# Performance work log

Hardware: AMD Instinct MI355X
Metric: run time of the kernel (lower is better)

The kernel has to match this reference:

```python
import jax, jax.numpy as jnp
import numpy as np

N = 16384       # pedestrian_num
D_IN = 2        # input_size
H = 64          # hidden_size


def setup_inputs() -> dict:
    key = jax.random.key(0)
    ks = jax.random.split(key, 4)
    data = jax.random.normal(ks[0], (N, D_IN), dtype=jnp.float32)
    # Linear weights stored as [in, out]; scaled like torch default init (~1/sqrt(in)).
    W1 = jax.random.normal(ks[1], (D_IN, 32), dtype=jnp.float32) / np.sqrt(D_IN)
    b1 = jnp.zeros((32,), dtype=jnp.float32)
    W2 = jax.random.normal(ks[2], (32, 64), dtype=jnp.float32) / np.sqrt(32)
    b2 = jnp.zeros((64,), dtype=jnp.float32)
    W3 = jax.random.normal(ks[3], (64, H), dtype=jnp.float32) / np.sqrt(64)
    b3 = jnp.zeros((H,), dtype=jnp.float32)
    return {"data": data, "W1": W1, "b1": b1, "W2": W2, "b2": b2, "W3": W3, "b3": b3}


def reference(data, W1, b1, W2, b2, W3, b3):
    # Per-pedestrian MLP (batched over all N pedestrians at once).
    h = jax.nn.relu(data @ W1 + b1)          # [N, 32]
    h = jax.nn.relu(h @ W2 + b2)             # [N, 64]
    h = h @ W3 + b3                          # [N, H]
    # Spatial affinity: the original fills the lower triangle with <h_i, h_j>
    # and its softmax reads entry [max(i,j), min(i,j)], i.e. the full
    # symmetric Gram matrix G = h @ h.T.
    G = jnp.einsum("nd,md->nm", h, h)        # [N, N], symmetric
    # Row-wise softmax over the symmetric affinity matrix.
    return jax.nn.softmax(G, axis=-1)
```

## Files before the change

### kernel.cpp

```cpp
#include <hip/hip_runtime.h>

#define N     16384
#define DH    64
#define TILE  128
#define NT    (N / TILE)
#define S2    133

typedef __attribute__((ext_vector_type(8))) short  short8;
typedef __attribute__((ext_vector_type(4))) float  f32x4;

__device__ __forceinline__ ushort bf_hi(float x) {
    unsigned u = __float_as_uint(x);
    unsigned r = u + 0x7FFFu + ((u >> 16) & 1u);
    return (ushort)(r >> 16);
}
__device__ __forceinline__ float bf_val(ushort h) {
    return __uint_as_float(((unsigned)h) << 16);
}

__device__ __forceinline__ short8 ldfrag(const ushort* __restrict__ p, int row, int koff) {
    return *(const short8*)(p + (size_t)row * DH + koff);
}

__global__ __launch_bounds__(128) void mlp_kernel(
    const float* __restrict__ data,
    const float* __restrict__ W1, const float* __restrict__ b1,
    const float* __restrict__ W2, const float* __restrict__ b2,
    const float* __restrict__ W3, const float* __restrict__ b3,
    ushort* __restrict__ hHi, ushort* __restrict__ hLo)
{
    __shared__ float sW1[64], sb1[32], sW2[32 * 64], sb2[64], sW3[64 * 64], sb3[64];
    const int tid = threadIdx.x;
    if (tid < 64) sW1[tid] = W1[tid];
    if (tid < 32) sb1[tid] = b1[tid];
    if (tid < 64) sb2[tid] = b2[tid];
    if (tid < 64) sb3[tid] = b3[tid];
    for (int t = tid; t < 32 * 64; t += 128) sW2[t] = W2[t];
    for (int t = tid; t < 64 * 64; t += 128) sW3[t] = W3[t];
    __syncthreads();

    const int i = blockIdx.x * 128 + tid;
    const float x0 = data[2 * i + 0];
    const float x1 = data[2 * i + 1];

    float h1[32];
#pragma unroll
    for (int o = 0; o < 32; ++o)
        h1[o] = fmaxf(0.f, fmaf(x0, sW1[o], fmaf(x1, sW1[32 + o], sb1[o])));

    float h2[64];
#pragma unroll
    for (int o = 0; o < 64; ++o) {
        float a = sb2[o];
#pragma unroll
        for (int k = 0; k < 32; ++k) a = fmaf(h1[k], sW2[k * 64 + o], a);
        h2[o] = fmaxf(0.f, a);
    }

    ushort hs[64], ls[64];
#pragma unroll
    for (int o = 0; o < 64; ++o) {
        float a = sb3[o];
#pragma unroll
        for (int k = 0; k < 64; ++k) a = fmaf(h2[k], sW3[k * 64 + o], a);
        const ushort hb = bf_hi(a);
        hs[o] = hb;
        ls[o] = bf_hi(a - bf_val(hb));
    }
#pragma unroll
    for (int q = 0; q < 8; ++q) {
        short8 vh, vl;
#pragma unroll
        for (int t = 0; t < 8; ++t) { vh[t] = (short)hs[q * 8 + t]; vl[t] = (short)ls[q * 8 + t]; }
        *(short8*)(hHi + (size_t)i * DH + q * 8) = vh;
        *(short8*)(hLo + (size_t)i * DH + q * 8) = vl;
    }
}

__device__ __forceinline__ void stage_B(
    const ushort* __restrict__ hHi, const ushort* __restrict__ hLo,
    int brow0, int tid, ushort* __restrict__ sB)
{
    const int arr = tid >> 7;
    const int r   = tid & 127;
    const ushort* __restrict__ src = (arr ? hLo : hHi) + (size_t)(brow0 + r) * DH;
    ushort* __restrict__ dst = sB + arr * (TILE * DH) + r * 64;
    const int sw = (r & 7);
#pragma unroll
    for (int q = 0; q < 8; ++q) {
        const short8 v = *(const short8*)(src + q * 8);
        *(short8*)(dst + 8 * (q ^ sw)) = v;
    }
}

__device__ __forceinline__ short8 ldB(const ushort* __restrict__ sB,
                                      int arr, int row, int ks, int kb)
{
    return *(const short8*)(sB + arr * (TILE * DH) + row * 64 + 8 * (((ks << 2) + kb) ^ (row & 7)));
}

__device__ __forceinline__ void gram_tile(
    const ushort* __restrict__ hHi, const ushort* __restrict__ hLo,
    const ushort* __restrict__ sB,
    int bi, int wave, int r16, int kb, f32x4 acc[2][8])
{
#pragma unroll
    for (int rb = 0; rb < 2; ++rb)
#pragma unroll
        for (int cb = 0; cb < 8; ++cb) acc[rb][cb] = (f32x4){0.f, 0.f, 0.f, 0.f};

    const int arow = bi * TILE + wave * 16 + r16;
#pragma unroll
    for (int ks = 0; ks < 2; ++ks) {
        const int koff = ks * 32 + kb * 8;
        const short8 Ah0 = ldfrag(hHi, arow,      koff);
        const short8 Ah1 = ldfrag(hHi, arow + 64, koff);
        const short8 Al0 = ldfrag(hLo, arow,      koff);
        const short8 Al1 = ldfrag(hLo, arow + 64, koff);
#pragma unroll
        for (int cb = 0; cb < 8; ++cb) {
            const int brow = cb * 16 + r16;
            const short8 Bh = ldB(sB, 0, brow, ks, kb);
            const short8 Bl = ldB(sB, 1, brow, ks, kb);
            acc[0][cb] = __builtin_amdgcn_mfma_f32_16x16x32_bf16(Ah0, Bh, acc[0][cb], 0, 0, 0);
            acc[0][cb] = __builtin_amdgcn_mfma_f32_16x16x32_bf16(Ah0, Bl, acc[0][cb], 0, 0, 0);
            acc[0][cb] = __builtin_amdgcn_mfma_f32_16x16x32_bf16(Al0, Bh, acc[0][cb], 0, 0, 0);
            acc[1][cb] = __builtin_amdgcn_mfma_f32_16x16x32_bf16(Ah1, Bh, acc[1][cb], 0, 0, 0);
            acc[1][cb] = __builtin_amdgcn_mfma_f32_16x16x32_bf16(Ah1, Bl, acc[1][cb], 0, 0, 0);
            acc[1][cb] = __builtin_amdgcn_mfma_f32_16x16x32_bf16(Al1, Bh, acc[1][cb], 0, 0, 0);
        }
    }
}

__device__ __forceinline__ int tile_row(int wave, int kb, int rb, int reg) {
    return rb * 64 + wave * 16 + kb * 4 + reg;
}

__device__ __forceinline__ void tri_decode(int p, int& bi, int& bj) {
    const int xcd = p & 7, s = p >> 3;
    const int q = s / 129, r = s % 129;
    const int P = xcd * 8 + q;
    if (r <= P) { bi = r;         bj = P;       }
    else        { bi = r - P - 1; bj = 127 - P; }
}

#define SMEM1_BYTES 32768

__global__ __launch_bounds__(256, 4) void pass1_mfma(
    const ushort* __restrict__ hHi, const ushort* __restrict__ hLo,
    float* __restrict__ part_m, float* __restrict__ part_l)
{
    int bi, bj;
    tri_decode(blockIdx.x, bi, bj);

    __shared__ __attribute__((aligned(16))) char smem[SMEM1_BYTES];
    ushort* sB = (ushort*)smem;
    float*  jm = (float*)smem;
    float*  jl = jm + 512;

    const int tid = threadIdx.x;
    const int wave = tid >> 6, lane = tid & 63;
    const int r16 = lane & 15, kb = lane >> 4;

    stage_B(hHi, hLo, bj * TILE, tid, sB);
    __syncthreads();

    f32x4 acc[2][8];
    gram_tile(hHi, hLo, sB, bi, wave, r16, kb, acc);

#pragma unroll
    for (int rb = 0; rb < 2; ++rb) {
#pragma unroll
        for (int reg = 0; reg < 4; ++reg) {
            float m = acc[rb][0][reg];
#pragma unroll
            for (int cb = 1; cb < 8; ++cb) m = fmaxf(m, acc[rb][cb][reg]);
            m = fmaxf(m, __shfl_xor(m, 1));
            m = fmaxf(m, __shfl_xor(m, 2));
            m = fmaxf(m, __shfl_xor(m, 4));
            m = fmaxf(m, __shfl_xor(m, 8));
            float sum = 0.f;
#pragma unroll
            for (int cb = 0; cb < 8; ++cb) sum += __expf(acc[rb][cb][reg] - m);
            sum += __shfl_xor(sum, 1);
            sum += __shfl_xor(sum, 2);
            sum += __shfl_xor(sum, 4);
            sum += __shfl_xor(sum, 8);
            if (r16 == 0) {
                const int grow = bi * TILE + tile_row(wave, kb, rb, reg);
                part_m[(size_t)bj * N + grow] = m;
                part_l[(size_t)bj * N + grow] = sum;
            }
        }
    }

    if (bi != bj) {
        __syncthreads();
#pragma unroll
        for (int cb = 0; cb < 8; ++cb) {
            float m = acc[0][cb][0];
#pragma unroll
            for (int rb = 0; rb < 2; ++rb)
#pragma unroll
                for (int reg = 0; reg < 4; ++reg) m = fmaxf(m, acc[rb][cb][reg]);
            m = fmaxf(m, __shfl_xor(m, 16));
            m = fmaxf(m, __shfl_xor(m, 32));
            float sum = 0.f;
#pragma unroll
            for (int rb = 0; rb < 2; ++rb)
#pragma unroll
                for (int reg = 0; reg < 4; ++reg) sum += __expf(acc[rb][cb][reg] - m);
            sum += __shfl_xor(sum, 16);
            sum += __shfl_xor(sum, 32);
            if (kb == 0) { jm[wave * 128 + cb * 16 + r16] = m; jl[wave * 128 + cb * 16 + r16] = sum; }
        }
        __syncthreads();
        if (tid < 128) {
            float M = jm[tid];
#pragma unroll
            for (int w = 1; w < 4; ++w) M = fmaxf(M, jm[w * 128 + tid]);
            float L = 0.f;
#pragma unroll
            for (int w = 0; w < 4; ++w) L += jl[w * 128 + tid] * __expf(jm[w * 128 + tid] - M);
            part_m[(size_t)bi * N + bj * TILE + tid] = M;
            part_l[(size_t)bi * N + bj * TILE + tid] = L;
        }
    }
}

__global__ __launch_bounds__(256) void merge_kernel(
    const float* __restrict__ part_m, const float* __restrict__ part_l,
    float* __restrict__ srow)
{
    const int i = blockIdx.x * 256 + threadIdx.x;
    float M = -3.0e38f;
    for (int o = 0; o < NT; ++o) M = fmaxf(M, part_m[(size_t)o * N + i]);
    float L = 0.f;
    for (int o = 0; o < NT; ++o)
        L = fmaf(part_l[(size_t)o * N + i], __expf(part_m[(size_t)o * N + i] - M), L);
    srow[i] = M + __logf(L);
}

__global__ __launch_bounds__(256, 2) void pass2_mfma(
    const ushort* __restrict__ hHi, const ushort* __restrict__ hLo,
    const float* __restrict__ srow,
    float* __restrict__ out)
{
    const int p = blockIdx.x;
    const int xcd = p & 7, slot = p >> 3;
    const int bj  = xcd * 16 + (slot & 15);
    const int bi0 = (slot >> 4) * 16;

    const int tid = threadIdx.x;
    const int wave = tid >> 6, lane = tid & 63;
    const int r16 = lane & 15, kb = lane >> 4;

    __shared__ __attribute__((aligned(16))) ushort sB[2 * TILE * DH];
    __shared__ float ldsP[64 * S2];

    stage_B(hHi, hLo, bj * TILE, tid, sB);
    __syncthreads();

    for (int it = 0; it < 16; ++it) {
        const int bi = bi0 + it;

        f32x4 acc[2][8];
        gram_tile(hHi, hLo, sB, bi, wave, r16, kb, acc);

#pragma unroll
        for (int hh = 0; hh < 2; ++hh) {
#pragma unroll
            for (int reg = 0; reg < 4; ++reg) {
                const int rl   = wave * 16 + kb * 4 + reg;
                const int grow = bi * TILE + hh * 64 + rl;
                const float s  = srow[grow];
#pragma unroll
                for (int cb = 0; cb < 8; ++cb)
                    ldsP[rl * S2 + cb * 16 + r16] = __expf(acc[hh][cb][reg] - s);
            }
            __syncthreads();
#pragma unroll
            for (int qq = 0; qq < 8; ++qq) {
                const int f4 = tid + 256 * qq;
                const int rl = f4 >> 5, c4 = f4 & 31;
                const f32x4 v = *(const f32x4*)&ldsP[rl * S2 + c4 * 4];
                f32x4* dst = (f32x4*)(out + (size_t)(bi * TILE + hh * 64 + rl) * N + bj * TILE + c4 * 4);
                __builtin_nontemporal_store(v, dst);
            }
            __syncthreads();
        }
    }
}

extern "C" void kernel_launch(void* const* d_in, const int* in_sizes, int n_in,
                              void* d_out, int out_size, void* d_ws, size_t ws_size,
                              hipStream_t stream)
{
    const float* data = (const float*)d_in[0];
    const float* W1   = (const float*)d_in[1];
    const float* b1   = (const float*)d_in[2];
    const float* W2   = (const float*)d_in[3];
    const float* b2   = (const float*)d_in[4];
    const float* W3   = (const float*)d_in[5];
    const float* b3   = (const float*)d_in[6];
    float* out = (float*)d_out;

    float* part_m = (float*)d_ws;
    float* part_l = part_m + (size_t)NT * N;
    float* srow   = part_l + (size_t)NT * N;
    ushort* hHi   = (ushort*)(srow + 2 * N);
    ushort* hLo   = hHi + (size_t)N * DH;

    mlp_kernel<<<N / 128, 128, 0, stream>>>(data, W1, b1, W2, b2, W3, b3, hHi, hLo);
    pass1_mfma<<<NT * (NT + 1) / 2, 256, 0, stream>>>(hHi, hLo, part_m, part_l);
    merge_kernel<<<N / 256, 256, 0, stream>>>(part_m, part_l, srow);
    pass2_mfma<<<1024, 256, 0, stream>>>(hHi, hLo, srow, out);
}
```

Measured before the change: 355.8 us.

## Compute full Gram grid in pass1 instead of exploiting symmetry

Pass1 no longer uses the symmetric upper-triangular tile decode, where each off-diagonal tile also produced column-wise softmax partials. Each block now keeps one staged B tile and loops over 16 row tiles, covering the full 128x128 tile grid with row-wise reductions only. This drops the extra shared-memory column reduction and its barriers, and B staging is amortized over 16 tiles. In exchange it roughly doubles the MFMA work in pass1.

```diff
diff --git a/kernel.cpp b/kernel.cpp
--- a/kernel.cpp
+++ b/kernel.cpp
@@ -136,94 +136,54 @@
     return rb * 64 + wave * 16 + kb * 4 + reg;
 }
 
-__device__ __forceinline__ void tri_decode(int p, int& bi, int& bj) {
-    const int xcd = p & 7, s = p >> 3;
-    const int q = s / 129, r = s % 129;
-    const int P = xcd * 8 + q;
-    if (r <= P) { bi = r;         bj = P;       }
-    else        { bi = r - P - 1; bj = 127 - P; }
-}
-
-#define SMEM1_BYTES 32768
-
 __global__ __launch_bounds__(256, 4) void pass1_mfma(
     const ushort* __restrict__ hHi, const ushort* __restrict__ hLo,
     float* __restrict__ part_m, float* __restrict__ part_l)
 {
-    int bi, bj;
-    tri_decode(blockIdx.x, bi, bj);
-
-    __shared__ __attribute__((aligned(16))) char smem[SMEM1_BYTES];
-    ushort* sB = (ushort*)smem;
-    float*  jm = (float*)smem;
-    float*  jl = jm + 512;
+    const int p = blockIdx.x;
+    const int xcd = p & 7, slot = p >> 3;
+    const int bj  = xcd * 16 + (slot & 15);
+    const int bi0 = (slot >> 4) * 16;
 
     const int tid = threadIdx.x;
     const int wave = tid >> 6, lane = tid & 63;
     const int r16 = lane & 15, kb = lane >> 4;
 
+    __shared__ __attribute__((aligned(16))) ushort sB[2 * TILE * DH];
+
     stage_B(hHi, hLo, bj * TILE, tid, sB);
     __syncthreads();
 
-    f32x4 acc[2][8];
-    gram_tile(hHi, hLo, sB, bi, wave, r16, kb, acc);
-
-#pragma unroll
-    for (int rb = 0; rb < 2; ++rb) {
-#pragma unroll
-        for (int reg = 0; reg < 4; ++reg) {
-            float m = acc[rb][0][reg];
-#pragma unroll
-            for (int cb = 1; cb < 8; ++cb) m = fmaxf(m, acc[rb][cb][reg]);
-            m = fmaxf(m, __shfl_xor(m, 1));
-            m = fmaxf(m, __shfl_xor(m, 2));
-            m = fmaxf(m, __shfl_xor(m, 4));
-            m = fmaxf(m, __shfl_xor(m, 8));
-            float sum = 0.f;
-#pragma unroll
-            for (int cb = 0; cb < 8; ++cb) sum += __expf(acc[rb][cb][reg] - m);
-            sum += __shfl_xor(sum, 1);
-            sum += __shfl_xor(sum, 2);
-            sum += __shfl_xor(sum, 4);
-            sum += __shfl_xor(sum, 8);
-            if (r16 == 0) {
-                const int grow = bi * TILE + tile_row(wave, kb, rb, reg);
-                part_m[(size_t)bj * N + grow] = m;
-                part_l[(size_t)bj * N + grow] = sum;
+    for (int it = 0; it < 16; ++it) {
+        const int bi = bi0 + it;
+
+        f32x4 acc[2][8];
+        gram_tile(hHi, hLo, sB, bi, wave, r16, kb, acc);
+
+#pragma unroll
+        for (int rb = 0; rb < 2; ++rb) {
+#pragma unroll
+            for (int e = 0; e < 4; ++e) {
+                float m = acc[rb][0][e];
+#pragma unroll
+                for (int cb = 1; cb < 8; ++cb) m = fmaxf(m, acc[rb][cb][e]);
+                m = fmaxf(m, __shfl_xor(m, 1));
+                m = fmaxf(m, __shfl_xor(m, 2));
+                m = fmaxf(m, __shfl_xor(m, 4));
+                m = fmaxf(m, __shfl_xor(m, 8));
+                float s = 0.f;
+#pragma unroll
+                for (int cb = 0; cb < 8; ++cb) s += __expf(acc[rb][cb][e] - m);
+                s += __shfl_xor(s, 1);
+                s += __shfl_xor(s, 2);
+                s += __shfl_xor(s, 4);
+                s += __shfl_xor(s, 8);
+                if (r16 == 0) {
+                    const int grow = bi * TILE + tile_row(wave, kb, rb, e);
+                    part_m[(size_t)bj * N + grow] = m;
+                    part_l[(size_t)bj * N + grow] = s;
+                }
             }
-        }
-    }
-
-    if (bi != bj) {
-        __syncthreads();
-#pragma unroll
-        for (int cb = 0; cb < 8; ++cb) {
-            float m = acc[0][cb][0];
-#pragma unroll
-            for (int rb = 0; rb < 2; ++rb)
-#pragma unroll
-                for (int reg = 0; reg < 4; ++reg) m = fmaxf(m, acc[rb][cb][reg]);
-            m = fmaxf(m, __shfl_xor(m, 16));
-            m = fmaxf(m, __shfl_xor(m, 32));
-            float sum = 0.f;
-#pragma unroll
-            for (int rb = 0; rb < 2; ++rb)
-#pragma unroll
-                for (int reg = 0; reg < 4; ++reg) sum += __expf(acc[rb][cb][reg] - m);
-            sum += __shfl_xor(sum, 16);
-            sum += __shfl_xor(sum, 32);
-            if (kb == 0) { jm[wave * 128 + cb * 16 + r16] = m; jl[wave * 128 + cb * 16 + r16] = sum; }
-        }
-        __syncthreads();
-        if (tid < 128) {
-            float M = jm[tid];
-#pragma unroll
-            for (int w = 1; w < 4; ++w) M = fmaxf(M, jm[w * 128 + tid]);
-            float L = 0.f;
-#pragma unroll
-            for (int w = 0; w < 4; ++w) L += jl[w * 128 + tid] * __expf(jm[w * 128 + tid] - M);
-            part_m[(size_t)bi * N + bj * TILE + tid] = M;
-            part_l[(size_t)bi * N + bj * TILE + tid] = L;
         }
     }
 }
@@ -312,7 +272,7 @@
     ushort* hLo   = hHi + (size_t)N * DH;
 
     mlp_kernel<<<N / 128, 128, 0, stream>>>(data, W1, b1, W2, b2, W3, b3, hHi, hLo);
-    pass1_mfma<<<NT * (NT + 1) / 2, 256, 0, stream>>>(hHi, hLo, part_m, part_l);
+    pass1_mfma<<<1024, 256, 0, stream>>>(hHi, hLo, part_m, part_l);
     merge_kernel<<<N / 256, 256, 0, stream>>>(part_m, part_l, srow);
     pass2_mfma<<<1024, 256, 0, stream>>>(hHi, hLo, srow, out);
 }
```

New measurement: 738.9 us. 108% more time.
